# Kernel optimization log

Hardware: AMD Instinct MI355X
Metric: run time of the kernel (lower is better)

Reference implementation:

```python
import jax, jax.numpy as jnp
import numpy as np

B, C, H, W = 4, 256, 64, 64
G = 32          # GroupNorm groups
EPS = 1e-6


def setup_inputs() -> dict:
    key = jax.random.key(0)
    ks = jax.random.split(key, 6)
    inp = {
        "x": jax.random.normal(ks[0], (B, C, H, W), dtype=jnp.float32),
        "gamma": jnp.ones((C,), jnp.float32),
        "beta": jnp.zeros((C,), jnp.float32),
        "wq": jax.random.normal(ks[1], (C, C), jnp.float32) * 0.02,
        "bq": jnp.zeros((C,), jnp.float32),
        "wk": jax.random.normal(ks[2], (C, C), jnp.float32) * 0.02,
        "bk": jnp.zeros((C,), jnp.float32),
        "wv": jax.random.normal(ks[3], (C, C), jnp.float32) * 0.02,
        "bv": jnp.zeros((C,), jnp.float32),
        "wp": jax.random.normal(ks[4], (C, C), jnp.float32) * 0.02,
        "bp": jnp.zeros((C,), jnp.float32),
    }
    return inp


def _group_norm(x, gamma, beta):
    b, c, h, w = x.shape
    xs = x.reshape(b, G, c // G, h, w)
    mu = xs.mean(axis=(2, 3, 4), keepdims=True)
    var = xs.var(axis=(2, 3, 4), keepdims=True)  # biased, matches torch GroupNorm
    xn = ((xs - mu) * jax.lax.rsqrt(var + EPS)).reshape(b, c, h, w)
    return xn * gamma[None, :, None, None] + beta[None, :, None, None]


def _conv1x1(s, w, bias):
    # 1x1 conv == per-pixel channel matmul
    return jnp.einsum('oc,bchw->bohw', w, s) + bias[None, :, None, None]


def reference(x, gamma, beta, wq, bq, wk, bk, wv, bv, wp, bp):
    b, c, h, w = x.shape
    s = _group_norm(x, gamma, beta)
    q = _conv1x1(s, wq, bq).reshape(b, c, h * w)  # [B, C, N]
    k = _conv1x1(s, wk, bk).reshape(b, c, h * w)
    v = _conv1x1(s, wv, bv).reshape(b, c, h * w)
    # scores[b,i,j] = sum_c q[b,c,i] k[b,c,j], scaled by C^-1/2
    scores = jnp.einsum('bci,bcj->bij', q, k) * (c ** -0.5)
    attn = jax.nn.softmax(scores, axis=2)
    # h_[b,c,i] = sum_j v[b,c,j] attn[b,i,j]
    h_ = jnp.einsum('bij,bcj->bci', attn, v).reshape(b, c, h, w)
    h_ = _conv1x1(h_, wp, bp)
    return x + h_
```

## Files before the change

### kernel.cpp

```cpp
#include <hip/hip_runtime.h>

#define BB 4
#define CCH 256
#define NPIX 4096
#define EPS 1e-6f

typedef __attribute__((ext_vector_type(8))) short bf16x8;
typedef __attribute__((ext_vector_type(4))) float f32x4;

__device__ __forceinline__ unsigned short f2bf(float f) {
    return (unsigned short)((__float_as_uint(f) + 0x8000u) >> 16);
}
__device__ __forceinline__ float bf2f(unsigned short h) {
    return __uint_as_float((unsigned)h << 16);
}
__device__ __forceinline__ void gl2lds16(const void* g, void* l) {
    __builtin_amdgcn_global_load_lds(
        (const __attribute__((address_space(1))) unsigned int*)g,
        (__attribute__((address_space(3))) unsigned int*)l, 16, 0, 0);
}

__global__ __launch_bounds__(256) void gn_apply(const float* __restrict__ x,
                                                const float* __restrict__ gamma,
                                                const float* __restrict__ beta,
                                                unsigned short* __restrict__ sb) {
    int bg = blockIdx.x;
    int b = bg >> 5, g = bg & 31;
    const float4* x4 = (const float4*)(x + (size_t)(b * CCH + g * 8) * NPIX);
    float s = 0.f, ss = 0.f;
    for (int e = threadIdx.x; e < 8 * NPIX / 4; e += 256) {
        float4 v = x4[e];
        s += v.x + v.y + v.z + v.w;
        ss += v.x * v.x + v.y * v.y + v.z * v.z + v.w * v.w;
    }
    __shared__ float rs[256], rss[256];
    __shared__ float mean_s, rstd_s;
    rs[threadIdx.x] = s; rss[threadIdx.x] = ss;
    __syncthreads();
    for (int off = 128; off > 0; off >>= 1) {
        if (threadIdx.x < (unsigned)off) {
            rs[threadIdx.x] += rs[threadIdx.x + off];
            rss[threadIdx.x] += rss[threadIdx.x + off];
        }
        __syncthreads();
    }
    if (threadIdx.x == 0) {
        const float inv = 1.0f / (float)(8 * NPIX);
        float m = rs[0] * inv;
        float var = rss[0] * inv - m * m;
        mean_s = m;
        rstd_s = rsqrtf(var + EPS);
    }
    __syncthreads();
    float scale[8], shift[8];
#pragma unroll
    for (int ci = 0; ci < 8; ++ci) {
        float ga = gamma[g * 8 + ci], be = beta[g * 8 + ci];
        scale[ci] = rstd_s * ga;
        shift[ci] = be - mean_s * scale[ci];
    }
#pragma unroll 1
    for (int r = 0; r < 4; ++r) {
        int pq = r * 256 + threadIdx.x;
        __align__(16) unsigned short h[4][8];
#pragma unroll
        for (int ci = 0; ci < 8; ++ci) {
            float4 v = x4[ci * 1024 + pq];
            h[0][ci] = f2bf(v.x * scale[ci] + shift[ci]);
            h[1][ci] = f2bf(v.y * scale[ci] + shift[ci]);
            h[2][ci] = f2bf(v.z * scale[ci] + shift[ci]);
            h[3][ci] = f2bf(v.w * scale[ci] + shift[ci]);
        }
        size_t base = ((size_t)(b * NPIX + pq * 4) << 8) + g * 8;
#pragma unroll
        for (int p = 0; p < 4; ++p)
            *(uint4*)(sb + base + (size_t)p * 256) = *(const uint4*)h[p];
    }
}

__global__ __launch_bounds__(256) void wcvt(const float* __restrict__ wq,
                                            const float* __restrict__ wk,
                                            const float* __restrict__ wv,
                                            const float* __restrict__ wp,
                                            unsigned short* __restrict__ wb) {
    int e = blockIdx.x * 256 + threadIdx.x;
    const float* srcs[4] = {wp, wq, wk, wv};
#pragma unroll
    for (int m = 0; m < 4; ++m) {
        float4 v = ((const float4*)srcs[m])[e];
        ushort4 h;
        h.x = f2bf(v.x); h.y = f2bf(v.y); h.z = f2bf(v.z); h.w = f2bf(v.w);
        *(ushort4*)(wb + (size_t)m * 65536 + (size_t)e * 4) = h;
    }
}

__global__ __launch_bounds__(256) void qkv_mfma(
    const unsigned short* __restrict__ sb, const unsigned short* __restrict__ wb,
    const float* __restrict__ bq, const float* __restrict__ bk,
    const float* __restrict__ bv,
    unsigned short* __restrict__ qT, unsigned short* __restrict__ kT,
    unsigned short* __restrict__ vB) {
    __shared__ __align__(16) char lds[34816];
    const int tid = threadIdx.x, lane = tid & 63, w = tid >> 6;
    const int ln15 = lane & 15, q = lane >> 4;
    const int n0 = blockIdx.x * 128;
    const int co0 = blockIdx.y * 128;
    const int z = blockIdx.z;
    const unsigned short* wm = wb + (size_t)(z + 1) * 65536;
    const float* bias = (z == 0) ? bq : (z == 1) ? bk : bv;

    f32x4 acc[2][8];
#pragma unroll
    for (int i2 = 0; i2 < 2; ++i2)
#pragma unroll
        for (int nf = 0; nf < 8; ++nf) {
            acc[i2][nf][0] = 0.f; acc[i2][nf][1] = 0.f;
            acc[i2][nf][2] = 0.f; acc[i2][nf][3] = 0.f;
        }

#pragma unroll 1
    for (int kt = 0; kt < 4; ++kt) {
#pragma unroll
        for (int r = 0; r < 4; ++r) {
            int gch = r * 256 + tid;
            int row = gch >> 3, sidx = gch & 7;
            int cc = sidx ^ (row & 7);
            gl2lds16(sb + ((size_t)(n0 + row) << 8) + kt * 64 + cc * 8,
                     &lds[r * 4096 + w * 1024]);
            gl2lds16(wm + ((size_t)(co0 + row) << 8) + kt * 64 + cc * 8,
                     &lds[16384 + r * 4096 + w * 1024]);
        }
        __syncthreads();
#pragma unroll
        for (int kk = 0; kk < 2; ++kk) {
            int kc = kk * 4 + q;
            bf16x8 af[2], bf[8];
#pragma unroll
            for (int i2 = 0; i2 < 2; ++i2) {
                int row = w * 32 + i2 * 16 + ln15;
                af[i2] = *(const bf16x8*)&lds[row * 128 + ((kc ^ (row & 7)) << 4)];
            }
#pragma unroll
            for (int nf = 0; nf < 8; ++nf) {
                int row = nf * 16 + ln15;
                bf[nf] = *(const bf16x8*)&lds[16384 + row * 128 + ((kc ^ (row & 7)) << 4)];
            }
#pragma unroll
            for (int i2 = 0; i2 < 2; ++i2)
#pragma unroll
                for (int nf = 0; nf < 8; ++nf)
                    acc[i2][nf] = __builtin_amdgcn_mfma_f32_16x16x32_bf16(
                        af[i2], bf[nf], acc[i2][nf], 0, 0, 0);
        }
        __syncthreads();
    }

    float bias_l[8];
#pragma unroll
    for (int nf = 0; nf < 8; ++nf) bias_l[nf] = bias[co0 + nf * 16 + ln15];
    const float scl = (z == 0) ? 0.0625f : 1.0f;
    unsigned short* T = (unsigned short*)lds;
    if (z < 2) {
#pragma unroll
        for (int i2 = 0; i2 < 2; ++i2)
#pragma unroll
            for (int nf = 0; nf < 8; ++nf)
#pragma unroll
                for (int r = 0; r < 4; ++r) {
                    int n_l = w * 32 + i2 * 16 + q * 4 + r;
                    int co_l = nf * 16 + ln15;
                    T[n_l * 136 + co_l] = f2bf((acc[i2][nf][r] + bias_l[nf]) * scl);
                }
    } else {
#pragma unroll
        for (int i2 = 0; i2 < 2; ++i2)
#pragma unroll
            for (int nf = 0; nf < 8; ++nf)
#pragma unroll
                for (int r = 0; r < 4; ++r) {
                    int n_l = w * 32 + i2 * 16 + q * 4 + r;
                    int co_l = nf * 16 + ln15;
                    T[co_l * 136 + n_l] = f2bf(acc[i2][nf][r] + bias_l[nf]);
                }
    }
    __syncthreads();
    int row = tid >> 1, half = tid & 1;
    const uint4* src = (const uint4*)&T[row * 136 + half * 64];
    uint4* dst;
    if (z < 2) {
        unsigned short* qk = (z == 0) ? qT : kT;
        dst = (uint4*)(qk + ((size_t)(n0 + row) << 8) + co0 + half * 64);
    } else {
        int b2 = n0 >> 12, pix0 = n0 & 4095;
        dst = (uint4*)(vB + ((size_t)(b2 * CCH + co0 + row) << 12) + pix0 + half * 64);
    }
#pragma unroll
    for (int u = 0; u < 8; ++u) dst[u] = src[u];
}

__global__ __launch_bounds__(256, 2) void attn_mfma(
    const unsigned short* __restrict__ qT, const unsigned short* __restrict__ kT,
    const unsigned short* __restrict__ vB,
    unsigned short* __restrict__ pO, float* __restrict__ pml) {
    __shared__ __align__(16) char lds[65536];
    const int tid = threadIdx.x, lane = tid & 63, w = tid >> 6;
    const int ln15 = lane & 15, q = lane >> 4;
    const int bx = blockIdx.x;
    const int jh = bx & 1, b = (bx >> 1) & 3;
    const int itile = bx >> 3;
    const int i0 = itile * 64;
    const int jbase = jh * 2048;
    const size_t nb = (size_t)b * NPIX;
    const int wslot = w * 2048;

#pragma unroll
    for (int t = 0; t < 8; ++t) {
        int gch = (w * 8 + t) * 64 + lane;
        int row = gch >> 5, sc = gch & 31;
        int cc = sc ^ (row & 7);
        gl2lds16(qT + ((nb + i0 + row) << 8) + cc * 8, &lds[(w * 8 + t) * 1024]);
    }
    __syncthreads();
    bf16x8 qf[8];
    {
        int row = w * 16 + ln15;
#pragma unroll
        for (int kb = 0; kb < 8; ++kb)
            qf[kb] = *(const bf16x8*)&lds[row * 512 + (((kb * 4 + q) ^ (row & 7)) << 4)];
    }
    __syncthreads();

    f32x4 O[16];
#pragma unroll
    for (int ns = 0; ns < 16; ++ns) {
        O[ns][0] = 0.f; O[ns][1] = 0.f; O[ns][2] = 0.f; O[ns][3] = 0.f;
    }
    float m_r[4], l_r[4];
#pragma unroll
    for (int r = 0; r < 4; ++r) { m_r[r] = -1e30f; l_r[r] = 0.f; }

#pragma unroll 1
    for (int jt = 0; jt < 32; ++jt) {
        const int j0 = jbase + jt * 64;
#pragma unroll
        for (int t = 0; t < 8; ++t) {
            int gch = (w * 8 + t) * 64 + lane;
            int row = gch >> 5, sc = gch & 31;
            int cc = sc ^ (row & 7);
            gl2lds16(kT + ((nb + j0 + row) << 8) + cc * 8, &lds[(w * 8 + t) * 1024]);
            int c = gch >> 3, sv = gch & 7;
            int jc = sv ^ (c & 7);
            gl2lds16(vB + ((size_t)(b * CCH + c) << 12) + j0 + jc * 8,
                     &lds[32768 + (w * 8 + t) * 1024]);
        }
        __syncthreads();

        f32x4 S[4];
#pragma unroll
        for (int js = 0; js < 4; ++js) {
            S[js][0] = 0.f; S[js][1] = 0.f; S[js][2] = 0.f; S[js][3] = 0.f;
        }
#pragma unroll
        for (int js = 0; js < 4; ++js) {
            int jr = js * 16 + ln15;
#pragma unroll
            for (int kb = 0; kb < 8; ++kb) {
                bf16x8 kf = *(const bf16x8*)&lds[jr * 512 + (((kb * 4 + q) ^ (jr & 7)) << 4)];
                S[js] = __builtin_amdgcn_mfma_f32_16x16x32_bf16(qf[kb], kf, S[js], 0, 0, 0);
            }
        }
        __syncthreads();

        float alpha[4];
#pragma unroll
        for (int r = 0; r < 4; ++r) {
            float s0 = S[0][r], s1 = S[1][r], s2 = S[2][r], s3 = S[3][r];
            float mx = fmaxf(fmaxf(s0, s1), fmaxf(s2, s3));
            mx = fmaxf(mx, __shfl_xor(mx, 1));
            mx = fmaxf(mx, __shfl_xor(mx, 2));
            mx = fmaxf(mx, __shfl_xor(mx, 4));
            mx = fmaxf(mx, __shfl_xor(mx, 8));
            float mo = m_r[r];
            float mn = fmaxf(mo, mx);
            float p0 = __expf(s0 - mn), p1 = __expf(s1 - mn);
            float p2 = __expf(s2 - mn), p3 = __expf(s3 - mn);
            float sm = p0 + p1 + p2 + p3;
            sm += __shfl_xor(sm, 1);
            sm += __shfl_xor(sm, 2);
            sm += __shfl_xor(sm, 4);
            sm += __shfl_xor(sm, 8);
            float al = __expf(mo - mn);
            m_r[r] = mn;
            l_r[r] = l_r[r] * al + sm;
            alpha[r] = al;
            int il = q * 4 + r;
            float pv[4] = {p0, p1, p2, p3};
#pragma unroll
            for (int js = 0; js < 4; ++js) {
                int j = js * 16 + ln15;
                *(unsigned short*)&lds[wslot + il * 128 +
                    (((j >> 3) ^ (il & 7)) << 4) + ((j & 7) << 1)] = f2bf(pv[js]);
            }
        }
        asm volatile("s_waitcnt lgkmcnt(0)" ::: "memory");

        bf16x8 pf[2];
#pragma unroll
        for (int kf2 = 0; kf2 < 2; ++kf2)
            pf[kf2] = *(const bf16x8*)&lds[wslot + ln15 * 128 +
                                           (((kf2 * 4 + q) ^ (ln15 & 7)) << 4)];
#pragma unroll
        for (int ns = 0; ns < 16; ++ns) {
            O[ns][0] *= alpha[0]; O[ns][1] *= alpha[1];
            O[ns][2] *= alpha[2]; O[ns][3] *= alpha[3];
        }
#pragma unroll
        for (int ns = 0; ns < 16; ++ns) {
            int c = ns * 16 + ln15;
            bf16x8 vf0 = *(const bf16x8*)&lds[32768 + c * 128 + ((q ^ (c & 7)) << 4)];
            bf16x8 vf1 = *(const bf16x8*)&lds[32768 + c * 128 + (((4 + q) ^ (c & 7)) << 4)];
            O[ns] = __builtin_amdgcn_mfma_f32_16x16x32_bf16(pf[0], vf0, O[ns], 0, 0, 0);
            O[ns] = __builtin_amdgcn_mfma_f32_16x16x32_bf16(pf[1], vf1, O[ns], 0, 0, 0);
        }
        __syncthreads();
    }

    size_t pbase = (size_t)bx * (64 * 256);
#pragma unroll
    for (int ns = 0; ns < 16; ++ns) {
        int c = ns * 16 + ln15;
#pragma unroll
        for (int r = 0; r < 4; ++r) {
            int i = w * 16 + q * 4 + r;
            pO[pbase + i * 256 + c] = f2bf(O[ns][r]);
        }
    }
    if (ln15 == 0) {
#pragma unroll
        for (int r = 0; r < 4; ++r) {
            int i = w * 16 + q * 4 + r;
            pml[bx * 128 + i] = m_r[r];
            pml[bx * 128 + 64 + i] = l_r[r];
        }
    }
}

__global__ __launch_bounds__(256) void attn_merge(
    const unsigned short* __restrict__ pO, const float* __restrict__ pml,
    unsigned short* __restrict__ hN) {
    int bid = blockIdx.x;
    int b = bid & 3, itile = bid >> 2;
    int bx0 = (itile << 3) | (b << 1), bx1 = bx0 | 1;
    __shared__ float f0s[64], f1s[64];
    int t = threadIdx.x;
    if (t < 64) {
        float m0 = pml[bx0 * 128 + t], l0 = pml[bx0 * 128 + 64 + t];
        float m1 = pml[bx1 * 128 + t], l1 = pml[bx1 * 128 + 64 + t];
        float ms = fmaxf(m0, m1);
        float e0 = __expf(m0 - ms), e1 = __expf(m1 - ms);
        float inv = 1.0f / (l0 * e0 + l1 * e1);
        f0s[t] = e0 * inv; f1s[t] = e1 * inv;
    }
    __syncthreads();
    const unsigned short* p0 = pO + (size_t)bx0 * 16384;
    const unsigned short* p1 = pO + (size_t)bx1 * 16384;
    int i = t >> 2, cq = t & 3;
    float f0 = f0s[i], f1 = f1s[i];
    size_t nrow = ((size_t)(b * NPIX + itile * 64 + i)) << 8;
#pragma unroll
    for (int p = 0; p < 16; ++p) {
        int c = p * 16 + cq * 4;
        ushort4 a = *(const ushort4*)&p0[i * 256 + c];
        ushort4 bb = *(const ushort4*)&p1[i * 256 + c];
        ushort4 h;
        h.x = f2bf(bf2f(a.x) * f0 + bf2f(bb.x) * f1);
        h.y = f2bf(bf2f(a.y) * f0 + bf2f(bb.y) * f1);
        h.z = f2bf(bf2f(a.z) * f0 + bf2f(bb.z) * f1);
        h.w = f2bf(bf2f(a.w) * f0 + bf2f(bb.w) * f1);
        *(ushort4*)&hN[nrow + c] = h;
    }
}

__global__ __launch_bounds__(256) void proj_mfma(
    const unsigned short* __restrict__ hN, const unsigned short* __restrict__ wb,
    const float* __restrict__ bp, const float* __restrict__ x,
    float* __restrict__ out) {
    __shared__ __align__(16) char lds[34816];
    const int tid = threadIdx.x, lane = tid & 63, w = tid >> 6;
    const int ln15 = lane & 15, q = lane >> 4;
    const int n0 = blockIdx.x * 128;
    const int co0 = blockIdx.y * 128;

    f32x4 acc[2][8];
#pragma unroll
    for (int i2 = 0; i2 < 2; ++i2)
#pragma unroll
        for (int nf = 0; nf < 8; ++nf) {
            acc[i2][nf][0] = 0.f; acc[i2][nf][1] = 0.f;
            acc[i2][nf][2] = 0.f; acc[i2][nf][3] = 0.f;
        }

#pragma unroll 1
    for (int kt = 0; kt < 4; ++kt) {
#pragma unroll
        for (int r = 0; r < 4; ++r) {
            int gch = r * 256 + tid;
            int row = gch >> 3, sidx = gch & 7;
            int cc = sidx ^ (row & 7);
            gl2lds16(hN + ((size_t)(n0 + row) << 8) + kt * 64 + cc * 8,
                     &lds[r * 4096 + w * 1024]);
            gl2lds16(wb + ((size_t)(co0 + row) << 8) + kt * 64 + cc * 8,
                     &lds[16384 + r * 4096 + w * 1024]);
        }
        __syncthreads();
#pragma unroll
        for (int kk = 0; kk < 2; ++kk) {
            int kc = kk * 4 + q;
            bf16x8 af[2], bf[8];
#pragma unroll
            for (int i2 = 0; i2 < 2; ++i2) {
                int row = w * 32 + i2 * 16 + ln15;
                af[i2] = *(const bf16x8*)&lds[row * 128 + ((kc ^ (row & 7)) << 4)];
            }
#pragma unroll
            for (int nf = 0; nf < 8; ++nf) {
                int row = nf * 16 + ln15;
                bf[nf] = *(const bf16x8*)&lds[16384 + row * 128 + ((kc ^ (row & 7)) << 4)];
            }
#pragma unroll
            for (int i2 = 0; i2 < 2; ++i2)
#pragma unroll
                for (int nf = 0; nf < 8; ++nf)
                    acc[i2][nf] = __builtin_amdgcn_mfma_f32_16x16x32_bf16(
                        af[i2], bf[nf], acc[i2][nf], 0, 0, 0);
        }
        __syncthreads();
    }

    unsigned short* T = (unsigned short*)lds;
#pragma unroll
    for (int i2 = 0; i2 < 2; ++i2)
#pragma unroll
        for (int nf = 0; nf < 8; ++nf)
#pragma unroll
            for (int r = 0; r < 4; ++r) {
                int n_l = w * 32 + i2 * 16 + q * 4 + r;
                int co_l = nf * 16 + ln15;
                T[co_l * 136 + n_l] = f2bf(acc[i2][nf][r]);
            }
    __syncthreads();
    int row = tid >> 1, half = tid & 1;
    int b2 = n0 >> 12, pix0 = n0 & 4095;
    float br = bp[co0 + row];
    size_t gidx = (((size_t)(b2 * CCH + co0 + row)) << 12) + pix0 + half * 64;
    const unsigned short* trow = &T[row * 136 + half * 64];
#pragma unroll
    for (int u = 0; u < 16; ++u) {
        float4 xv = *(const float4*)&x[gidx + u * 4];
        ushort4 tv = *(const ushort4*)&trow[u * 4];
        float4 o;
        o.x = xv.x + br + bf2f(tv.x);
        o.y = xv.y + br + bf2f(tv.y);
        o.z = xv.z + br + bf2f(tv.z);
        o.w = xv.w + br + bf2f(tv.w);
        *(float4*)&out[gidx + u * 4] = o;
    }
}

extern "C" void kernel_launch(void* const* d_in, const int* in_sizes, int n_in,
                              void* d_out, int out_size, void* d_ws, size_t ws_size,
                              hipStream_t stream) {
    const float* x     = (const float*)d_in[0];
    const float* gamma = (const float*)d_in[1];
    const float* beta  = (const float*)d_in[2];
    const float* wq    = (const float*)d_in[3];
    const float* bq    = (const float*)d_in[4];
    const float* wk    = (const float*)d_in[5];
    const float* bk    = (const float*)d_in[6];
    const float* wv    = (const float*)d_in[7];
    const float* bv    = (const float*)d_in[8];
    const float* wp    = (const float*)d_in[9];
    const float* bp    = (const float*)d_in[10];
    float* out = (float*)d_out;

    char* wsb = (char*)d_ws;
    unsigned short* sb  = (unsigned short*)wsb;
    unsigned short* hN  = sb;
    unsigned short* wb  = (unsigned short*)(wsb + 8388608);
    unsigned short* pO  = (unsigned short*)(wsb + 8912896);
    float*          pml = (float*)(wsb + 25690112);
    unsigned short* qT  = (unsigned short*)(wsb + 25952256);
    unsigned short* kT  = (unsigned short*)(wsb + 34340864);
    unsigned short* vB  = (unsigned short*)(wsb + 42729472);

    gn_apply<<<BB * 32, 256, 0, stream>>>(x, gamma, beta, sb);
    wcvt<<<64, 256, 0, stream>>>(wq, wk, wv, wp, wb);
    qkv_mfma<<<dim3(128, 2, 3), 256, 0, stream>>>(sb, wb, bq, bk, bv, qT, kT, vB);
    attn_mfma<<<512, 256, 0, stream>>>(qT, kT, vB, pO, pml);
    attn_merge<<<256, 256, 0, stream>>>(pO, pml, hN);
    proj_mfma<<<dim3(128, 2), 256, 0, stream>>>(hN, wb, bp, x, out);
}
```

Before: 260.7 us.

## Software-pipeline K/V tile loads with split waits in attention kernel

```diff
diff --git a/kernel.cpp b/kernel.cpp
--- a/kernel.cpp
+++ b/kernel.cpp
@@ -202,7 +202,7 @@
     const unsigned short* __restrict__ qT, const unsigned short* __restrict__ kT,
     const unsigned short* __restrict__ vB,
     unsigned short* __restrict__ pO, float* __restrict__ pml) {
-    __shared__ __align__(16) char lds[65536];
+    __shared__ __align__(16) char lds[73728];
     const int tid = threadIdx.x, lane = tid & 63, w = tid >> 6;
     const int ln15 = lane & 15, q = lane >> 4;
     const int bx = blockIdx.x;
@@ -211,7 +211,7 @@
     const int i0 = itile * 64;
     const int jbase = jh * 2048;
     const size_t nb = (size_t)b * NPIX;
-    const int wslot = w * 2048;
+    const int wslot = 65536 + w * 2048;
 
 #pragma unroll
     for (int t = 0; t < 8; ++t) {
@@ -239,37 +239,59 @@
 #pragma unroll
     for (int r = 0; r < 4; ++r) { m_r[r] = -1e30f; l_r[r] = 0.f; }
 
-#pragma unroll 1
-    for (int jt = 0; jt < 32; ++jt) {
-        const int j0 = jbase + jt * 64;
+    {
+        const int j0 = jbase;
 #pragma unroll
         for (int t = 0; t < 8; ++t) {
             int gch = (w * 8 + t) * 64 + lane;
             int row = gch >> 5, sc = gch & 31;
             int cc = sc ^ (row & 7);
             gl2lds16(kT + ((nb + j0 + row) << 8) + cc * 8, &lds[(w * 8 + t) * 1024]);
+        }
+#pragma unroll
+        for (int t = 0; t < 8; ++t) {
+            int gch = (w * 8 + t) * 64 + lane;
             int c = gch >> 3, sv = gch & 7;
             int jc = sv ^ (c & 7);
             gl2lds16(vB + ((size_t)(b * CCH + c) << 12) + j0 + jc * 8,
                      &lds[32768 + (w * 8 + t) * 1024]);
         }
-        __syncthreads();
+    }
+
+#pragma unroll 1
+    for (int jt = 0; jt < 32; ++jt) {
+        asm volatile("s_waitcnt vmcnt(8)" ::: "memory");
+        __builtin_amdgcn_s_barrier();
 
         f32x4 S[4];
 #pragma unroll
         for (int js = 0; js < 4; ++js) {
             S[js][0] = 0.f; S[js][1] = 0.f; S[js][2] = 0.f; S[js][3] = 0.f;
         }
-#pragma unroll
-        for (int js = 0; js < 4; ++js) {
-            int jr = js * 16 + ln15;
-#pragma unroll
-            for (int kb = 0; kb < 8; ++kb) {
+        __builtin_amdgcn_s_setprio(1);
+#pragma unroll
+        for (int kb = 0; kb < 8; ++kb)
+#pragma unroll
+            for (int js = 0; js < 4; ++js) {
+                int jr = js * 16 + ln15;
                 bf16x8 kf = *(const bf16x8*)&lds[jr * 512 + (((kb * 4 + q) ^ (jr & 7)) << 4)];
                 S[js] = __builtin_amdgcn_mfma_f32_16x16x32_bf16(qf[kb], kf, S[js], 0, 0, 0);
             }
-        }
-        __syncthreads();
+        __builtin_amdgcn_s_setprio(0);
+
+        asm volatile("" ::: "memory");
+        __builtin_amdgcn_s_barrier();
+        if (jt < 31) {
+            const int j0n = jbase + (jt + 1) * 64;
+#pragma unroll
+            for (int t = 0; t < 8; ++t) {
+                int gch = (w * 8 + t) * 64 + lane;
+                int row = gch >> 5, sc = gch & 31;
+                int cc = sc ^ (row & 7);
+                gl2lds16(kT + ((nb + j0n + row) << 8) + cc * 8,
+                         &lds[(w * 8 + t) * 1024]);
+            }
+        }
 
         float alpha[4];
 #pragma unroll
@@ -314,6 +336,15 @@
             O[ns][0] *= alpha[0]; O[ns][1] *= alpha[1];
             O[ns][2] *= alpha[2]; O[ns][3] *= alpha[3];
         }
+
+        if (jt < 31) {
+            asm volatile("s_waitcnt vmcnt(8)" ::: "memory");
+        } else {
+            asm volatile("s_waitcnt vmcnt(0)" ::: "memory");
+        }
+        __builtin_amdgcn_s_barrier();
+
+        __builtin_amdgcn_s_setprio(1);
 #pragma unroll
         for (int ns = 0; ns < 16; ++ns) {
             int c = ns * 16 + ln15;
@@ -322,7 +353,21 @@
             O[ns] = __builtin_amdgcn_mfma_f32_16x16x32_bf16(pf[0], vf0, O[ns], 0, 0, 0);
             O[ns] = __builtin_amdgcn_mfma_f32_16x16x32_bf16(pf[1], vf1, O[ns], 0, 0, 0);
         }
-        __syncthreads();
+        __builtin_amdgcn_s_setprio(0);
+
+        asm volatile("" ::: "memory");
+        __builtin_amdgcn_s_barrier();
+        if (jt < 31) {
+            const int j0n = jbase + (jt + 1) * 64;
+#pragma unroll
+            for (int t = 0; t < 8; ++t) {
+                int gch = (w * 8 + t) * 64 + lane;
+                int c = gch >> 3, sv = gch & 7;
+                int jc = sv ^ (c & 7);
+                gl2lds16(vB + ((size_t)(b * CCH + c) << 12) + j0n + jc * 8,
+                         &lds[32768 + (w * 8 + t) * 1024]);
+            }
+        }
     }
 
     size_t pbase = (size_t)bx * (64 * 256);
```

New measurement: 269.4 us. 3.3% more time.
